# Performance work log

Measured on AMD Instinct MI355X. Metric: run time of the kernel, lower is better.

## Reference

```python
import jax, jax.numpy as jnp
import numpy as np

B, N, NODE_DIM = 256, 200, 2
H, D, L, FF = 8, 128, 3, 512
KD = D // H  # key/val dim per head = 16
EPS = 1e-5


def _uniform(key, shape, fan):
    s = 1.0 / np.sqrt(fan)
    return jax.random.uniform(key, shape, jnp.float32, -s, s)


def setup_inputs() -> dict:
    key = jax.random.key(0)
    ks = jax.random.split(key, 16)
    return {
        "x": jax.random.normal(ks[0], (B, N, NODE_DIM), jnp.float32),
        "Wemb": _uniform(ks[1], (NODE_DIM, D), NODE_DIM),
        "bemb": _uniform(ks[2], (D,), NODE_DIM),
        "Wq": _uniform(ks[3], (L, H, D, KD), KD),
        "Wk": _uniform(ks[4], (L, H, D, KD), KD),
        "Wv": _uniform(ks[5], (L, H, D, KD), KD),
        "Wo": _uniform(ks[6], (L, H, KD, D), D),
        "bn1_g": jnp.ones((L, D), jnp.float32),
        "bn1_b": jnp.zeros((L, D), jnp.float32),
        "W1": _uniform(ks[7], (L, D, FF), D),
        "b1": _uniform(ks[8], (L, FF), D),
        "W2": _uniform(ks[9], (L, FF, D), FF),
        "b2": _uniform(ks[10], (L, D), FF),
        "bn2_g": jnp.ones((L, D), jnp.float32),
        "bn2_b": jnp.zeros((L, D), jnp.float32),
    }


def _batch_norm(h, g, b):
    # BatchNorm1d in training mode: stats over all (batch*graph) positions per channel
    hf = h.reshape(-1, h.shape[-1])
    m = hf.mean(axis=0)
    v = hf.var(axis=0)  # biased variance, as torch uses for normalization
    return (h - m) * jax.lax.rsqrt(v + EPS) * g + b


def _mha(h, Wq, Wk, Wv, Wo):
    # h: [B,N,D]; Wq/Wk/Wv: [H,D,KD]; Wo: [H,KD,D]
    Q = jnp.einsum('bnd,hdk->hbnk', h, Wq)
    K = jnp.einsum('bnd,hdk->hbnk', h, Wk)
    V = jnp.einsum('bnd,hdk->hbnk', h, Wv)
    scores = jnp.einsum('hbqk,hbnk->hbqn', Q, K) * (1.0 / np.sqrt(KD))
    attn = jax.nn.softmax(scores, axis=-1)
    heads = jnp.einsum('hbqn,hbnk->hbqk', attn, V)
    return jnp.einsum('hbqk,hkd->bqd', heads, Wo)


def reference(x, Wemb, bemb, Wq, Wk, Wv, Wo, bn1_g, bn1_b, W1, b1, W2, b2, bn2_g, bn2_b):
    h = x @ Wemb + bemb  # init_embed: [B,N,D]
    for l in range(L):
        h = h + _mha(h, Wq[l], Wk[l], Wv[l], Wo[l])
        h = _batch_norm(h, bn1_g[l], bn1_b[l])
        ff = jax.nn.relu(h @ W1[l] + b1[l]) @ W2[l] + b2[l]
        h = _batch_norm(h + ff, bn2_g[l], bn2_b[l])
    return (h, h.mean(axis=1))
```

## Files before the change

kernel.cpp:

```cpp
#include <hip/hip_runtime.h>
#include <math.h>

#define B_ 256
#define N_ 200
#define D_ 128
#define H_ 8
#define KD_ 16
#define L_ 3
#define FF_ 512
#define ROWS (B_*N_)
#define BND (ROWS*D_)

typedef float f32x4 __attribute__((ext_vector_type(4)));
typedef _Float16 f16x4 __attribute__((ext_vector_type(4)));
typedef _Float16 f16x8 __attribute__((ext_vector_type(8)));

__device__ __forceinline__ ushort f2h_bits(float f) {
  _Float16 h = (_Float16)f;
  union { _Float16 h; ushort u; } v; v.h = h; return v.u;
}
__device__ __forceinline__ float h2f(ushort u) {
  union { ushort u; _Float16 h; } v; v.u = u; return (float)v.h;
}
__device__ __forceinline__ void splith(float f, ushort& hi, ushort& lo) {
  _Float16 h = (_Float16)f;
  float hf = (float)h;
  _Float16 l = (_Float16)(f - hf);
  union { _Float16 h; ushort u; } a, b; a.h = h; b.h = l;
  hi = a.u; lo = b.u;
}

__global__ __launch_bounds__(256) void embed_kernel(const float* __restrict__ x,
    const float* __restrict__ Wemb, const float* __restrict__ bemb,
    ushort* __restrict__ hhi, ushort* __restrict__ hlo)
{
  int i4 = blockIdx.x * 256 + threadIdx.x;
  int r  = i4 >> 5, c4 = i4 & 31;
  float x0 = x[2*r], x1 = x[2*r + 1];
  const float4 w0 = ((const float4*)Wemb)[c4];
  const float4 w1 = ((const float4*)Wemb)[32 + c4];
  const float4 bb = ((const float4*)bemb)[c4];
  float o[4];
  o[0] = fmaf(x0, w0.x, fmaf(x1, w1.x, bb.x));
  o[1] = fmaf(x0, w0.y, fmaf(x1, w1.y, bb.y));
  o[2] = fmaf(x0, w0.z, fmaf(x1, w1.z, bb.z));
  o[3] = fmaf(x0, w0.w, fmaf(x1, w1.w, bb.w));
  ushort hi[4], lo[4];
#pragma unroll
  for (int k = 0; k < 4; k++) splith(o[k], hi[k], lo[k]);
  uint2 ph, pl;
  ph.x = (uint)hi[0] | ((uint)hi[1] << 16);
  ph.y = (uint)hi[2] | ((uint)hi[3] << 16);
  pl.x = (uint)lo[0] | ((uint)lo[1] << 16);
  pl.y = (uint)lo[2] | ((uint)lo[3] << 16);
  ((uint2*)hhi)[i4] = ph;
  ((uint2*)hlo)[i4] = pl;
}

__global__ __launch_bounds__(256) void t_wo(const float* __restrict__ Wo,
    ushort* __restrict__ dh)
{
  int i = blockIdx.x * 256 + threadIdx.x;
  int l = i / 16384, r = i % 16384;
  int n = r >> 7, k = r & 127;
  int hh = k >> 4, kd = k & 15;
  float w = Wo[l*16384 + hh*2048 + kd*128 + n];
  dh[i] = f2h_bits(w);
}
__global__ __launch_bounds__(256) void t_w2(const float* __restrict__ W2,
    ushort* __restrict__ dh)
{
  int i = blockIdx.x * 256 + threadIdx.x;
  int l = i / 65536, r = i % 65536;
  int d = r >> 9, f = r & 511;
  float w = W2[l*65536 + f*128 + d];
  dh[i] = f2h_bits(w);
}

__global__ __launch_bounds__(128) void init_scales(float* __restrict__ sc, float* __restrict__ sh)
{
  int c = threadIdx.x;
  sc[c] = 1.f;
  sh[c] = 0.f;
}

__global__ __launch_bounds__(128) void fold_qkv(const float* __restrict__ Wq,
    const float* __restrict__ Wk, const float* __restrict__ Wv,
    const float* __restrict__ sc, const float* __restrict__ sh,
    ushort* __restrict__ wh, float* __restrict__ bout)
{
  __shared__ float wsum[2];
  int n = blockIdx.x;
  int k = threadIdx.x;
  int which = n >> 7, hh = (n >> 4) & 7, kd = n & 15;
  const float* src = (which == 0) ? Wq : (which == 1) ? Wk : Wv;
  float w = src[hh*2048 + k*16 + kd];
  if (which == 0) w *= 0.25f * 1.44269504088896340736f;
  wh[n*128 + k] = f2h_bits(w * sc[k]);
  float p = sh[k] * w;
#pragma unroll
  for (int d = 1; d < 64; d <<= 1) p += __shfl_xor(p, d);
  if ((k & 63) == 0) wsum[k >> 6] = p;
  __syncthreads();
  if (k == 0) bout[n] = wsum[0] + wsum[1];
}

__global__ __launch_bounds__(128) void fold_w1(const float* __restrict__ W1,
    const float* __restrict__ b1, const float* __restrict__ sc, const float* __restrict__ sh,
    ushort* __restrict__ wh, float* __restrict__ bout)
{
  __shared__ float wsum[2];
  int f = blockIdx.x;
  int k = threadIdx.x;
  float w = W1[k*512 + f];
  wh[f*128 + k] = f2h_bits(w * sc[k]);
  float p = sh[k] * w;
#pragma unroll
  for (int d = 1; d < 64; d <<= 1) p += __shfl_xor(p, d);
  if ((k & 63) == 0) wsum[k >> 6] = p;
  __syncthreads();
  if (k == 0) bout[f] = b1[f] + wsum[0] + wsum[1];
}

template<int K, bool ALO, bool BIAS, bool RELU, bool RESIDBN,
         bool OUTQKV, bool OUT16, bool OUTHL, bool STATS>
__global__ __launch_bounds__(256, 2) void gemm_mfma(
    const ushort* __restrict__ Ahi, const ushort* __restrict__ Alo,
    const ushort* __restrict__ Wh,
    const float* __restrict__ bias,
    const ushort* rhi, const ushort* rlo,
    const float* __restrict__ rsc, const float* __restrict__ rsh,
    ushort* o0, ushort* o1, ushort* o2, ushort* o3,
    float* __restrict__ psum, float* __restrict__ psq, int Ntot)
{
  __shared__ ushort AhiS[128*64];
  __shared__ ushort AloS[ALO ? 128*64 : 8];
  __shared__ ushort BhS [128*64];
  const int t    = threadIdx.x;
  const int nx   = gridDim.x;
  const int nwg  = nx * gridDim.y;
  const int lin  = blockIdx.y * nx + blockIdx.x;
  const int q8   = nwg >> 3, r8 = nwg & 7;
  const int xcd  = lin & 7, i8 = lin >> 3;
  const int wg   = (xcd < r8 ? xcd*(q8+1) : r8*(q8+1) + (xcd-r8)*q8) + i8;
  const int bm   = (wg / nx) * 128;
  const int bn   = (wg % nx) * 128;
  const int lane = t & 63;
  const int w    = t >> 6, wm = w >> 1, wn = w & 1;
  const int quad = lane >> 4, l15 = lane & 15;
  const int bky  = wg / nx;

  f32x4 acc[4][4];
#pragma unroll
  for (int i = 0; i < 4; i++)
#pragma unroll
    for (int j = 0; j < 4; j++) acc[i][j] = (f32x4){0.f, 0.f, 0.f, 0.f};

  const ushort* AhiB = Ahi + (size_t)bm * K;
  const ushort* AloB = ALO ? (Alo + (size_t)bm * K) : nullptr;
  const ushort* BhB  = Wh  + (size_t)bn * K;

  for (int k0 = 0; k0 < K; k0 += 64) {
#pragma unroll
    for (int i = 0; i < 4; i++) {
      int idx = i * 256 + t;
      int row = idx >> 3, c = idx & 7;
      int k8  = c ^ (row & 7);
      size_t off = (size_t)row * K + k0 + k8 * 8;
      ((uint4*)AhiS)[idx] = *(const uint4*)(AhiB + off);
      if (ALO) ((uint4*)AloS)[idx] = *(const uint4*)(AloB + off);
      ((uint4*)BhS)[idx]  = *(const uint4*)(BhB + off);
    }
    __syncthreads();
#pragma unroll
    for (int ks = 0; ks < 2; ks++) {
      f16x8 ah[4], al[4], bh[4];
#pragma unroll
      for (int i = 0; i < 4; i++) {
        int row = wm * 64 + i * 16 + l15;
        int k8  = ks * 4 + quad;
        int ci  = k8 ^ (row & 7);
        ah[i] = ((const f16x8*)AhiS)[row * 8 + ci];
        if (ALO) al[i] = ((const f16x8*)AloS)[row * 8 + ci];
        int nrow = wn * 64 + i * 16 + l15;
        int cj   = k8 ^ (nrow & 7);
        bh[i] = ((const f16x8*)BhS)[nrow * 8 + cj];
      }
#pragma unroll
      for (int i = 0; i < 4; i++)
#pragma unroll
        for (int j = 0; j < 4; j++) {
          if (ALO) acc[i][j] = __builtin_amdgcn_mfma_f32_16x16x32_f16(al[i], bh[j], acc[i][j], 0, 0, 0);
          acc[i][j] = __builtin_amdgcn_mfma_f32_16x16x32_f16(ah[i], bh[j], acc[i][j], 0, 0, 0);
        }
    }
    __syncthreads();
  }

  float bv[4], scv[4], shv[4];
#pragma unroll
  for (int j = 0; j < 4; j++) {
    int col = bn + wn*64 + j*16 + l15;
    if (BIAS)    bv[j]  = bias[col];
    if (RESIDBN) { scv[j] = rsc[col]; shv[j] = rsh[col]; }
  }
  float sj[4] = {0.f,0.f,0.f,0.f}, qj[4] = {0.f,0.f,0.f,0.f};
#pragma unroll
  for (int i = 0; i < 4; i++) {
#pragma unroll
    for (int r = 0; r < 4; r++) {
      int row = bm + wm*64 + i*16 + quad*4 + r;
#pragma unroll
      for (int j = 0; j < 4; j++) {
        int col = bn + wn*64 + j*16 + l15;
        float v = acc[i][j][r];
        if (BIAS)    v += bv[j];
        if (RELU)    v = fmaxf(v, 0.f);
        if (RESIDBN) {
          size_t ri = (size_t)row * Ntot + col;
          float rr = h2f(rhi[ri]) + h2f(rlo[ri]);
          v += fmaf(rr, scv[j], shv[j]);
        }
        if (OUTQKV) {
          if (bn == 0) {
            o0[((size_t)(col >> 4) * ROWS + row) * 16 + (col & 15)] = f2h_bits(v);
          } else if (bn == 128) {
            int c = col - 128;
            o1[((size_t)(c >> 4) * ROWS + row) * 16 + (c & 15)] = f2h_bits(v);
          } else {
            int c = col - 256;
            ushort hi, lo; splith(v, hi, lo);
            size_t oi = ((size_t)(c >> 4) * ROWS + row) * 16 + (c & 15);
            o2[oi] = hi;
            o3[oi] = lo;
          }
        }
        if (OUT16) o0[(size_t)row * Ntot + col] = f2h_bits(v);
        if (OUTHL) {
          ushort hi, lo; splith(v, hi, lo);
          o0[(size_t)row * Ntot + col] = hi;
          o1[(size_t)row * Ntot + col] = lo;
        }
        if (STATS) { sj[j] += v; qj[j] = fmaf(v, v, qj[j]); }
      }
    }
  }
  if (STATS) {
#pragma unroll
    for (int j = 0; j < 4; j++) {
      sj[j] += __shfl_xor(sj[j], 16); sj[j] += __shfl_xor(sj[j], 32);
      qj[j] += __shfl_xor(qj[j], 16); qj[j] += __shfl_xor(qj[j], 32);
    }
    float* ssum = (float*)AhiS;
    float* ssq  = ssum + 128;
    if (t < 128) { ssum[t] = 0.f; ssq[t] = 0.f; }
    __syncthreads();
    if (quad == 0) {
#pragma unroll
      for (int j = 0; j < 4; j++) {
        int col = wn*64 + j*16 + l15;
        atomicAdd(&ssum[col], sj[j]);
        atomicAdd(&ssq[col],  qj[j]);
      }
    }
    __syncthreads();
    if (t < 128) {
      psum[bky * 128 + t] = ssum[t];
      psq [bky * 128 + t] = ssq[t];
    }
  }
}

__global__ __launch_bounds__(256) void attn_kernel(const ushort* __restrict__ qs,
    const ushort* __restrict__ ks, const ushort* __restrict__ vh,
    const ushort* __restrict__ vl, ushort* __restrict__ hd)
{
  __shared__ __align__(16) _Float16 Ksh[208*24];
  __shared__ __align__(16) _Float16 VTh[16*216];
  __shared__ __align__(16) _Float16 VTl[16*216];
  const int b  = blockIdx.x >> 3;
  const int hh = blockIdx.x & 7;
  const int t  = threadIdx.x;
  const size_t rb = (size_t)b * N_;
  const size_t hb = ((size_t)hh * ROWS + rb) * 16;

  for (int i = t; i < 208*2; i += 256) {
    int n = i >> 1, half = i & 1;
    uint4 kv = {0u, 0u, 0u, 0u};
    if (n < N_) kv = *(const uint4*)(ks + hb + n*16 + half*8);
    *(uint4*)&Ksh[n*24 + half*8] = kv;
  }
  for (int i = t; i < 208*2; i += 256) {
    int n = i >> 1, half = i & 1;
    uint4 v0 = {0u, 0u, 0u, 0u}, v1 = {0u, 0u, 0u, 0u};
    if (n < N_) {
      v0 = *(const uint4*)(vh + hb + n*16 + half*8);
      v1 = *(const uint4*)(vl + hb + n*16 + half*8);
    }
    const ushort* e0 = (const ushort*)&v0;
    const ushort* e1 = (const ushort*)&v1;
#pragma unroll
    for (int q = 0; q < 8; q++) {
      ((ushort*)VTh)[(half*8 + q)*216 + n] = e0[q];
      ((ushort*)VTl)[(half*8 + q)*216 + n] = e1[q];
    }
  }
  __syncthreads();

  const int lane = t & 63;
  const int w    = t >> 6;
  const int l15  = lane & 15;
  const int g    = lane >> 4;

  for (int qt = w; qt < 13; qt += 4) {
    int qr  = qt*16 + l15;
    int qrc = qr < N_ ? qr : N_-1;
    f16x4 bq = *(const f16x4*)(qs + hb + (size_t)qrc*16 + g*4);

    f32x4 ct[13];
#pragma unroll
    for (int kt = 0; kt < 13; kt++) {
      f16x4 ak = *(const f16x4*)&Ksh[(kt*16 + l15)*24 + g*4];
      ct[kt] = __builtin_amdgcn_mfma_f32_16x16x16f16(ak, bq, (f32x4){0.f,0.f,0.f,0.f}, 0, 0, 0);
    }
#pragma unroll
    for (int r = 0; r < 4; r++)
      if (g*4 + r >= 8) ct[12][r] = -1e30f;

    float m0 = -1e30f, m1 = -1e30f;
#pragma unroll
    for (int kt = 0; kt < 13; kt++) {
      m0 = fmaxf(m0, fmaxf(ct[kt][0], ct[kt][1]));
      m1 = fmaxf(m1, fmaxf(ct[kt][2], ct[kt][3]));
    }
    float m = fmaxf(m0, m1);
    m = fmaxf(m, __shfl_xor(m, 16));
    m = fmaxf(m, __shfl_xor(m, 32));

    float la0 = 0.f, la1 = 0.f, la2 = 0.f, la3 = 0.f;
#pragma unroll
    for (int kt = 0; kt < 13; kt++) {
      float p0 = __builtin_amdgcn_exp2f(ct[kt][0] - m);
      float p1 = __builtin_amdgcn_exp2f(ct[kt][1] - m);
      float p2 = __builtin_amdgcn_exp2f(ct[kt][2] - m);
      float p3 = __builtin_amdgcn_exp2f(ct[kt][3] - m);
      la0 += p0; la1 += p1; la2 += p2; la3 += p3;
      ct[kt][0] = p0; ct[kt][1] = p1; ct[kt][2] = p2; ct[kt][3] = p3;
    }
    float l = (la0 + la1) + (la2 + la3);
    l += __shfl_xor(l, 16);
    l += __shfl_xor(l, 32);

    f32x4 och = {0.f,0.f,0.f,0.f}, ocl = {0.f,0.f,0.f,0.f};
#pragma unroll
    for (int kt = 0; kt < 13; kt++) {
      f16x4 pt = { (_Float16)ct[kt][0], (_Float16)ct[kt][1],
                   (_Float16)ct[kt][2], (_Float16)ct[kt][3] };
      f16x4 avh = *(const f16x4*)&VTh[l15*216 + kt*16 + g*4];
      f16x4 avl = *(const f16x4*)&VTl[l15*216 + kt*16 + g*4];
      och = __builtin_amdgcn_mfma_f32_16x16x16f16(avh, pt, och, 0, 0, 0);
      ocl = __builtin_amdgcn_mfma_f32_16x16x16f16(avl, pt, ocl, 0, 0, 0);
    }

    if (qr < N_) {
      float inv = __builtin_amdgcn_rcpf(l);
      ushort o16[4];
#pragma unroll
      for (int r = 0; r < 4; r++) o16[r] = f2h_bits((och[r] + ocl[r]) * inv);
      uint2 p;
      p.x = (uint)o16[0] | ((uint)o16[1] << 16);
      p.y = (uint)o16[2] | ((uint)o16[3] << 16);
      *(uint2*)(hd + (rb + qr)*128 + hh*16 + g*4) = p;
    }
  }
}

__global__ __launch_bounds__(64) void bn_finalize(const float* __restrict__ psum,
    const float* __restrict__ psq, const float* __restrict__ g,
    const float* __restrict__ bta, float* __restrict__ scale, float* __restrict__ shift)
{
  int c = blockIdx.x;
  int i = threadIdx.x;
  float s = 0.f, q = 0.f;
  for (int r = i; r < 400; r += 64) { s += psum[r*128 + c]; q += psq[r*128 + c]; }
#pragma unroll
  for (int d = 32; d > 0; d >>= 1) { s += __shfl_down(s, d); q += __shfl_down(q, d); }
  if (i == 0) {
    const float invM = 1.f / 51200.f;
    float m  = s * invM;
    float v  = fmaf(q, invM, -m * m);
    float r  = rsqrtf(v + 1e-5f);
    float sc = r * g[c];
    scale[c] = sc;
    shift[c] = fmaf(-m, sc, bta[c]);
  }
}

__global__ __launch_bounds__(128) void bn_mean_final(const ushort* __restrict__ hhi,
    const ushort* __restrict__ hlo,
    const float* __restrict__ scale, const float* __restrict__ shift,
    float* __restrict__ outh, float* __restrict__ mout)
{
  int b = blockIdx.x, d = threadIdx.x;
  float sc = scale[d], sh = shift[d];
  float s = 0.f;
  for (int n = 0; n < N_; n++) {
    size_t idx = ((size_t)b * N_ + n) * 128 + d;
    float v = fmaf(h2f(hhi[idx]) + h2f(hlo[idx]), sc, sh);
    outh[idx] = v;
    s += v;
  }
  mout[b * 128 + d] = s * (1.f / N_);
}

extern "C" void kernel_launch(void* const* d_in, const int* in_sizes, int n_in,
                              void* d_out, int out_size, void* d_ws, size_t ws_size,
                              hipStream_t stream)
{
  const float* x    = (const float*)d_in[0];
  const float* Wemb = (const float*)d_in[1];
  const float* bemb = (const float*)d_in[2];
  const float* Wq   = (const float*)d_in[3];
  const float* Wk   = (const float*)d_in[4];
  const float* Wv   = (const float*)d_in[5];
  const float* Wo   = (const float*)d_in[6];
  const float* bn1g = (const float*)d_in[7];
  const float* bn1b = (const float*)d_in[8];
  const float* W1   = (const float*)d_in[9];
  const float* b1   = (const float*)d_in[10];
  const float* W2   = (const float*)d_in[11];
  const float* b2   = (const float*)d_in[12];
  const float* bn2g = (const float*)d_in[13];
  const float* bn2b = (const float*)d_in[14];
  float* out = (float*)d_out;

  char* wsb = (char*)d_ws;
  ushort* h_hi  = (ushort*)wsb;
  ushort* h_lo  = (ushort*)(wsb + 13107200);
  char*   phase = wsb + 26214400;
  ushort* qsb   = (ushort*)phase;
  ushort* ksb   = (ushort*)(phase + 13107200);
  ushort* vhh   = (ushort*)(phase + 26214400);
  ushort* vll   = (ushort*)(phase + 39321600);
  ushort* hd    = (ushort*)(phase + 52428800);
  ushort* hid   = (ushort*)phase;
  char*   wp    = wsb + 91750400;
  ushort* woT   = (ushort*)wp;
  ushort* w2T   = (ushort*)(wp + 98304);
  ushort* fqkvw = (ushort*)(wp + 491520);
  ushort* fw1w  = (ushort*)(wp + 589824);
  float*  fqkv_b = (float*)(wp + 720896);
  float*  fw1_b  = (float*)(wp + 722432);
  float*  psum   = (float*)(wp + 724480);
  float*  psq    = (float*)(wp + 929280);
  float*  sc_a   = (float*)(wp + 1134080);
  float*  sh_a   = (float*)(wp + 1134592);
  float*  sc_b   = (float*)(wp + 1135104);
  float*  sh_b   = (float*)(wp + 1135616);

  embed_kernel<<<6400, 256, 0, stream>>>(x, Wemb, bemb, h_hi, h_lo);
  t_wo<<<192, 256, 0, stream>>>(Wo, woT);
  t_w2<<<768, 256, 0, stream>>>(W2, w2T);
  init_scales<<<1, 128, 0, stream>>>(sc_b, sh_b);

  for (int l = 0; l < L_; l++) {
    fold_qkv<<<384, 128, 0, stream>>>(Wq + l*16384, Wk + l*16384, Wv + l*16384,
                                      sc_b, sh_b, fqkvw, fqkv_b);
    gemm_mfma<128, true, true, false, false, true, false, false, false>
        <<<dim3(3, 400), 256, 0, stream>>>(
        h_hi, h_lo, fqkvw, fqkv_b, nullptr, nullptr, nullptr, nullptr,
        qsb, ksb, vhh, vll, nullptr, nullptr, 384);
    attn_kernel<<<B_ * H_, 256, 0, stream>>>(qsb, ksb, vhh, vll, hd);
    gemm_mfma<128, false, false, false, true, false, false, true, true>
        <<<dim3(1, 400), 256, 0, stream>>>(
        hd, nullptr, woT + l*16384, nullptr, h_hi, h_lo, sc_b, sh_b,
        h_hi, h_lo, nullptr, nullptr, psum, psq, 128);
    bn_finalize<<<128, 64, 0, stream>>>(psum, psq, bn1g + l*128, bn1b + l*128, sc_a, sh_a);
    fold_w1<<<512, 128, 0, stream>>>(W1 + l*65536, b1 + l*512, sc_a, sh_a, fw1w, fw1_b);
    gemm_mfma<128, true, true, true, false, false, true, false, false>
        <<<dim3(4, 400), 256, 0, stream>>>(
        h_hi, h_lo, fw1w, fw1_b, nullptr, nullptr, nullptr, nullptr,
        hid, nullptr, nullptr, nullptr, nullptr, nullptr, 512);
    gemm_mfma<512, false, true, false, true, false, false, true, true>
        <<<dim3(1, 400), 256, 0, stream>>>(
        hid, nullptr, w2T + l*65536, b2 + l*128, h_hi, h_lo, sc_a, sh_a,
        h_hi, h_lo, nullptr, nullptr, psum, psq, 128);
    bn_finalize<<<128, 64, 0, stream>>>(psum, psq, bn2g + l*128, bn2b + l*128, sc_b, sh_b);
  }

  bn_mean_final<<<B_, 128, 0, stream>>>(h_hi, h_lo, sc_b, sh_b, out, out + BND);
}
```

Before: 610.2 us.

## Drop V low-half precision split and fold BN finalize into consumer kernels

V is now stored and multiplied in a single fp16 buffer instead of hi/lo split halves. This halves V traffic and the PV MFMAs in the attention kernel, at some cost in accuracy. The separate bn_finalize and init_scales launches are removed. Instead, each thread of fold_qkv, fold_w1 and bn_mean_final serially reduces the 400 partial sums, which saves launches but repeats that reduction in every block.

```diff
diff --git a/kernel.cpp b/kernel.cpp
--- a/kernel.cpp
+++ b/kernel.cpp
@@ -28,6 +28,18 @@
   _Float16 l = (_Float16)(f - hf);
   union { _Float16 h; ushort u; } a, b; a.h = h; b.h = l;
   hi = a.u; lo = b.u;
+}
+__device__ __forceinline__ void bn_reduce(const float* psum, const float* psq,
+    const float* gamma, const float* beta, int c, float& sc, float& sh) {
+  if (gamma == nullptr) { sc = 1.f; sh = 0.f; return; }
+  float s = 0.f, q = 0.f;
+  for (int r = 0; r < 400; r++) { s += psum[r*128 + c]; q += psq[r*128 + c]; }
+  const float invM = 1.f / 51200.f;
+  float m = s * invM;
+  float v = fmaf(q, invM, -m * m);
+  float rr = rsqrtf(v + 1e-5f);
+  sc = rr * gamma[c];
+  sh = fmaf(-m, sc, beta[c]);
 }
 
 __global__ __launch_bounds__(256) void embed_kernel(const float* __restrict__ x,
@@ -77,27 +89,25 @@
   dh[i] = f2h_bits(w);
 }
 
-__global__ __launch_bounds__(128) void init_scales(float* __restrict__ sc, float* __restrict__ sh)
-{
-  int c = threadIdx.x;
-  sc[c] = 1.f;
-  sh[c] = 0.f;
-}
-
 __global__ __launch_bounds__(128) void fold_qkv(const float* __restrict__ Wq,
     const float* __restrict__ Wk, const float* __restrict__ Wv,
-    const float* __restrict__ sc, const float* __restrict__ sh,
-    ushort* __restrict__ wh, float* __restrict__ bout)
+    const float* __restrict__ psum, const float* __restrict__ psq,
+    const float* __restrict__ gamma, const float* __restrict__ beta,
+    ushort* __restrict__ wh, float* __restrict__ bout,
+    float* __restrict__ scout, float* __restrict__ shout)
 {
   __shared__ float wsum[2];
   int n = blockIdx.x;
   int k = threadIdx.x;
+  float sc, sh;
+  bn_reduce(psum, psq, gamma, beta, k, sc, sh);
+  if (n == 0) { scout[k] = sc; shout[k] = sh; }
   int which = n >> 7, hh = (n >> 4) & 7, kd = n & 15;
   const float* src = (which == 0) ? Wq : (which == 1) ? Wk : Wv;
   float w = src[hh*2048 + k*16 + kd];
   if (which == 0) w *= 0.25f * 1.44269504088896340736f;
-  wh[n*128 + k] = f2h_bits(w * sc[k]);
-  float p = sh[k] * w;
+  wh[n*128 + k] = f2h_bits(w * sc);
+  float p = sh * w;
 #pragma unroll
   for (int d = 1; d < 64; d <<= 1) p += __shfl_xor(p, d);
   if ((k & 63) == 0) wsum[k >> 6] = p;
@@ -106,15 +116,21 @@
 }
 
 __global__ __launch_bounds__(128) void fold_w1(const float* __restrict__ W1,
-    const float* __restrict__ b1, const float* __restrict__ sc, const float* __restrict__ sh,
-    ushort* __restrict__ wh, float* __restrict__ bout)
+    const float* __restrict__ b1,
+    const float* __restrict__ psum, const float* __restrict__ psq,
+    const float* __restrict__ gamma, const float* __restrict__ beta,
+    ushort* __restrict__ wh, float* __restrict__ bout,
+    float* __restrict__ scout, float* __restrict__ shout)
 {
   __shared__ float wsum[2];
   int f = blockIdx.x;
   int k = threadIdx.x;
+  float sc, sh;
+  bn_reduce(psum, psq, gamma, beta, k, sc, sh);
+  if (f == 0) { scout[k] = sc; shout[k] = sh; }
   float w = W1[k*512 + f];
-  wh[f*128 + k] = f2h_bits(w * sc[k]);
-  float p = sh[k] * w;
+  wh[f*128 + k] = f2h_bits(w * sc);
+  float p = sh * w;
 #pragma unroll
   for (int d = 1; d < 64; d <<= 1) p += __shfl_xor(p, d);
   if ((k & 63) == 0) wsum[k >> 6] = p;
@@ -130,7 +146,7 @@
     const float* __restrict__ bias,
     const ushort* rhi, const ushort* rlo,
     const float* __restrict__ rsc, const float* __restrict__ rsh,
-    ushort* o0, ushort* o1, ushort* o2, ushort* o3,
+    ushort* o0, ushort* o1, ushort* o2,
     float* __restrict__ psum, float* __restrict__ psq, int Ntot)
 {
   __shared__ ushort AhiS[128*64];
@@ -229,10 +245,7 @@
             o1[((size_t)(c >> 4) * ROWS + row) * 16 + (c & 15)] = f2h_bits(v);
           } else {
             int c = col - 256;
-            ushort hi, lo; splith(v, hi, lo);
-            size_t oi = ((size_t)(c >> 4) * ROWS + row) * 16 + (c & 15);
-            o2[oi] = hi;
-            o3[oi] = lo;
+            o2[((size_t)(c >> 4) * ROWS + row) * 16 + (c & 15)] = f2h_bits(v);
           }
         }
         if (OUT16) o0[(size_t)row * Ntot + col] = f2h_bits(v);
@@ -273,11 +286,10 @@
 
 __global__ __launch_bounds__(256) void attn_kernel(const ushort* __restrict__ qs,
     const ushort* __restrict__ ks, const ushort* __restrict__ vh,
-    const ushort* __restrict__ vl, ushort* __restrict__ hd)
+    ushort* __restrict__ hd)
 {
   __shared__ __align__(16) _Float16 Ksh[208*24];
   __shared__ __align__(16) _Float16 VTh[16*216];
-  __shared__ __align__(16) _Float16 VTl[16*216];
   const int b  = blockIdx.x >> 3;
   const int hh = blockIdx.x & 7;
   const int t  = threadIdx.x;
@@ -292,18 +304,12 @@
   }
   for (int i = t; i < 208*2; i += 256) {
     int n = i >> 1, half = i & 1;
-    uint4 v0 = {0u, 0u, 0u, 0u}, v1 = {0u, 0u, 0u, 0u};
-    if (n < N_) {
-      v0 = *(const uint4*)(vh + hb + n*16 + half*8);
-      v1 = *(const uint4*)(vl + hb + n*16 + half*8);
-    }
+    uint4 v0 = {0u, 0u, 0u, 0u};
+    if (n < N_) v0 = *(const uint4*)(vh + hb + n*16 + half*8);
     const ushort* e0 = (const ushort*)&v0;
-    const ushort* e1 = (const ushort*)&v1;
-#pragma unroll
-    for (int q = 0; q < 8; q++) {
+#pragma unroll
+    for (int q = 0; q < 8; q++)
       ((ushort*)VTh)[(half*8 + q)*216 + n] = e0[q];
-      ((ushort*)VTl)[(half*8 + q)*216 + n] = e1[q];
-    }
   }
   __syncthreads();
 
@@ -351,22 +357,20 @@
     l += __shfl_xor(l, 16);
     l += __shfl_xor(l, 32);
 
-    f32x4 och = {0.f,0.f,0.f,0.f}, ocl = {0.f,0.f,0.f,0.f};
+    f32x4 och = {0.f,0.f,0.f,0.f};
 #pragma unroll
     for (int kt = 0; kt < 13; kt++) {
       f16x4 pt = { (_Float16)ct[kt][0], (_Float16)ct[kt][1],
                    (_Float16)ct[kt][2], (_Float16)ct[kt][3] };
       f16x4 avh = *(const f16x4*)&VTh[l15*216 + kt*16 + g*4];
-      f16x4 avl = *(const f16x4*)&VTl[l15*216 + kt*16 + g*4];
       och = __builtin_amdgcn_mfma_f32_16x16x16f16(avh, pt, och, 0, 0, 0);
-      ocl = __builtin_amdgcn_mfma_f32_16x16x16f16(avl, pt, ocl, 0, 0, 0);
     }
 
     if (qr < N_) {
       float inv = __builtin_amdgcn_rcpf(l);
       ushort o16[4];
 #pragma unroll
-      for (int r = 0; r < 4; r++) o16[r] = f2h_bits((och[r] + ocl[r]) * inv);
+      for (int r = 0; r < 4; r++) o16[r] = f2h_bits(och[r] * inv);
       uint2 p;
       p.x = (uint)o16[0] | ((uint)o16[1] << 16);
       p.y = (uint)o16[2] | ((uint)o16[3] << 16);
@@ -375,34 +379,15 @@
   }
 }
 
-__global__ __launch_bounds__(64) void bn_finalize(const float* __restrict__ psum,
-    const float* __restrict__ psq, const float* __restrict__ g,
-    const float* __restrict__ bta, float* __restrict__ scale, float* __restrict__ shift)
-{
-  int c = blockIdx.x;
-  int i = threadIdx.x;
-  float s = 0.f, q = 0.f;
-  for (int r = i; r < 400; r += 64) { s += psum[r*128 + c]; q += psq[r*128 + c]; }
-#pragma unroll
-  for (int d = 32; d > 0; d >>= 1) { s += __shfl_down(s, d); q += __shfl_down(q, d); }
-  if (i == 0) {
-    const float invM = 1.f / 51200.f;
-    float m  = s * invM;
-    float v  = fmaf(q, invM, -m * m);
-    float r  = rsqrtf(v + 1e-5f);
-    float sc = r * g[c];
-    scale[c] = sc;
-    shift[c] = fmaf(-m, sc, bta[c]);
-  }
-}
-
 __global__ __launch_bounds__(128) void bn_mean_final(const ushort* __restrict__ hhi,
     const ushort* __restrict__ hlo,
-    const float* __restrict__ scale, const float* __restrict__ shift,
+    const float* __restrict__ psum, const float* __restrict__ psq,
+    const float* __restrict__ gamma, const float* __restrict__ beta,
     float* __restrict__ outh, float* __restrict__ mout)
 {
   int b = blockIdx.x, d = threadIdx.x;
-  float sc = scale[d], sh = shift[d];
+  float sc, sh;
+  bn_reduce(psum, psq, gamma, beta, d, sc, sh);
   float s = 0.f;
   for (int n = 0; n < N_; n++) {
     size_t idx = ((size_t)b * N_ + n) * 128 + d;
@@ -441,7 +426,6 @@
   ushort* qsb   = (ushort*)phase;
   ushort* ksb   = (ushort*)(phase + 13107200);
   ushort* vhh   = (ushort*)(phase + 26214400);
-  ushort* vll   = (ushort*)(phase + 39321600);
   ushort* hd    = (ushort*)(phase + 52428800);
   ushort* hid   = (ushort*)phase;
   char*   wp    = wsb + 91750400;
@@ -461,32 +445,35 @@
   embed_kernel<<<6400, 256, 0, stream>>>(x, Wemb, bemb, h_hi, h_lo);
   t_wo<<<192, 256, 0, stream>>>(Wo, woT);
   t_w2<<<768, 256, 0, stream>>>(W2, w2T);
-  init_scales<<<1, 128, 0, stream>>>(sc_b, sh_b);
 
   for (int l = 0; l < L_; l++) {
     fold_qkv<<<384, 128, 0, stream>>>(Wq + l*16384, Wk + l*16384, Wv + l*16384,
-                                      sc_b, sh_b, fqkvw, fqkv_b);
+                                      psum, psq,
+                                      l == 0 ? nullptr : bn2g + (l-1)*128,
+                                      l == 0 ? nullptr : bn2b + (l-1)*128,
+                                      fqkvw, fqkv_b, sc_b, sh_b);
     gemm_mfma<128, true, true, false, false, true, false, false, false>
         <<<dim3(3, 400), 256, 0, stream>>>(
         h_hi, h_lo, fqkvw, fqkv_b, nullptr, nullptr, nullptr, nullptr,
-        qsb, ksb, vhh, vll, nullptr, nullptr, 384);
-    attn_kernel<<<B_ * H_, 256, 0, stream>>>(qsb, ksb, vhh, vll, hd);
+        qsb, ksb, vhh, nullptr, nullptr, 384);
+    attn_kernel<<<B_ * H_, 256, 0, stream>>>(qsb, ksb, vhh, hd);
     gemm_mfma<128, false, false, false, true, false, false, true, true>
         <<<dim3(1, 400), 256, 0, stream>>>(
         hd, nullptr, woT + l*16384, nullptr, h_hi, h_lo, sc_b, sh_b,
-        h_hi, h_lo, nullptr, nullptr, psum, psq, 128);
-    bn_finalize<<<128, 64, 0, stream>>>(psum, psq, bn1g + l*128, bn1b + l*128, sc_a, sh_a);
-    fold_w1<<<512, 128, 0, stream>>>(W1 + l*65536, b1 + l*512, sc_a, sh_a, fw1w, fw1_b);
+        h_hi, h_lo, nullptr, psum, psq, 128);
+    fold_w1<<<512, 128, 0, stream>>>(W1 + l*65536, b1 + l*512,
+                                     psum, psq, bn1g + l*128, bn1b + l*128,
+                                     fw1w, fw1_b, sc_a, sh_a);
     gemm_mfma<128, true, true, true, false, false, true, false, false>
         <<<dim3(4, 400), 256, 0, stream>>>(
         h_hi, h_lo, fw1w, fw1_b, nullptr, nullptr, nullptr, nullptr,
-        hid, nullptr, nullptr, nullptr, nullptr, nullptr, 512);
+        hid, nullptr, nullptr, nullptr, nullptr, 512);
     gemm_mfma<512, false, true, false, true, false, false, true, true>
         <<<dim3(1, 400), 256, 0, stream>>>(
         hid, nullptr, w2T + l*65536, b2 + l*128, h_hi, h_lo, sc_a, sh_a,
-        h_hi, h_lo, nullptr, nullptr, psum, psq, 128);
-    bn_finalize<<<128, 64, 0, stream>>>(psum, psq, bn2g + l*128, bn2b + l*128, sc_b, sh_b);
-  }
-
-  bn_mean_final<<<B_, 128, 0, stream>>>(h_hi, h_lo, sc_b, sh_b, out, out + BND);
-}
+        h_hi, h_lo, nullptr, psum, psq, 128);
+  }
+
+  bn_mean_final<<<B_, 128, 0, stream>>>(h_hi, h_lo, psum, psq,
+                                        bn2g + 2*128, bn2b + 2*128, out, out + BND);
+}
```

New measurement: 624.1 us. 2.3% more time.
